# Kernel optimization log

Measured on AMD Instinct MI355X. Metric: run time of the kernel, lower is better.

Reference implementation:

```python
import jax, jax.numpy as jnp
import numpy as np

DIM_X = 128
DIM_H = 128
HIDDEN = 512
BATCH = 4096


def _vf(x, h, t, W1, b1, W2, b2):
    # cfg vector field: 2-layer tanh MLP on concat([x, h, t]) -> (B, dim_x)
    B = x.shape[0]
    tcol = jnp.broadcast_to(jnp.reshape(t, (1, 1)), (B, 1)).astype(x.dtype)
    z = jnp.concatenate([x, h, tcol], axis=-1)  # (B, dim_x+dim_h+1)
    return jnp.tanh(z @ W1 + b1) @ W2 + b2  # (B, dim_x)


def _divergence(x, h, t, W1, b1, W2, b2):
    # Exact Jacobian trace: sum_i d v_i / d x_i, via dim_x forward-mode JVP
    # passes (replaces the torch per-dim reverse-mode autograd.grad loop).
    f = lambda xx: _vf(xx, h, t, W1, b1, W2, b2)
    dim = x.shape[1]

    def diag_i(i):
        e = jnp.zeros((dim,), x.dtype).at[i].set(1.0)
        _, tang = jax.jvp(f, (x,), (jnp.broadcast_to(e, x.shape),))  # (B, dim)
        return jnp.take(tang, i, axis=1)  # (B,)

    diag = jax.vmap(diag_i)(jnp.arange(dim))  # (dim, B)
    return jnp.sum(diag, axis=0)[:, None]  # (B, 1)


def setup_inputs() -> dict:
    key = jax.random.key(0)
    ks = jax.random.split(key, 9)
    return {
        "state": jax.random.normal(ks[0], (BATCH, DIM_X + 1), jnp.float32),
        "h": jax.random.normal(ks[1], (BATCH, DIM_H), jnp.float32),
        "h_null": jax.random.normal(ks[2], (BATCH, DIM_H), jnp.float32),
        "t": jax.random.uniform(ks[3], (1,), jnp.float32),
        "guidance_scale": jax.random.uniform(ks[4], (1,), jnp.float32),
        "W1": jax.random.normal(ks[5], (DIM_X + DIM_H + 1, HIDDEN), jnp.float32) * 0.05,
        "b1": jax.random.normal(ks[6], (HIDDEN,), jnp.float32) * 0.05,
        "W2": jax.random.normal(ks[7], (HIDDEN, DIM_X), jnp.float32) * 0.05,
        "b2": jax.random.normal(ks[8], (DIM_X,), jnp.float32) * 0.05,
    }


def reference(state, h, h_null, t, guidance_scale, W1, b1, W2, b2):
    x_t = state[:, :-1]  # (B, dim_x)
    gs = guidance_scale[0]
    v_h = _vf(x_t, h, t, W1, b1, W2, b2)
    v_h_null = _vf(x_t, h_null, t, W1, b1, W2, b2)
    v = (1.0 - gs) * v_h_null + gs * v_h
    div_h = _divergence(x_t, h, t, W1, b1, W2, b2)
    div_h_null = _divergence(x_t, h_null, t, W1, b1, W2, b2)
    div = (1.0 - gs) * div_h_null + gs * div_h
    return jnp.concatenate([v, div], axis=1)  # (B, dim_x+1)
```

## Files before the change

### kernel.cpp

```cpp
#include <hip/hip_runtime.h>
#include <hip/hip_bf16.h>

#define DX 128
#define DH 128
#define HID 512
#define NB 4096
#define ROWS 16
#define OUTC 129

typedef __attribute__((ext_vector_type(4))) float f32x4;
typedef __attribute__((ext_vector_type(2))) float float2v;
typedef __attribute__((ext_vector_type(8))) short bf16x8;
typedef __attribute__((ext_vector_type(2))) short bf16x2;

__device__ inline short f2bf(float f) {
    unsigned u = __float_as_uint(f);
    unsigned r = (u + 0x7fffu + ((u >> 16) & 1u)) >> 16;
    return (short)r;
}

__device__ inline float fast_tanh(float x) {
    float e = __expf(2.0f * x);
    float r = __builtin_amdgcn_rcpf(e + 1.0f);
    return 1.0f - 2.0f * r;
}

__global__ __launch_bounds__(256) void prep_kernel(
    const float* __restrict__ W1, const float* __restrict__ W2,
    float* __restrict__ c, short* __restrict__ w1p, short* __restrict__ w2p)
{
    __shared__ float tile[4][32][17];

    const int tid  = threadIdx.x;
    const int lane = tid & 63;
    const int w    = tid >> 6;
    const int l15  = lane & 15;
    const int l4   = lane >> 4;
    const int W    = blockIdx.x * 4 + w;

    if (W < 256) {
        int nt = W >> 3, ks = W & 7;
        int m0 = ks * 32, n0 = nt * 16;
        #pragma unroll
        for (int p = 0; p < 8; ++p) {
            int r = p * 4 + l4;
            tile[w][r][l15] = W1[(m0 + r) * HID + n0 + l15];
        }
    } else if (W < 384) {
        int idx = W - 256;
        int nt = idx >> 4, ks = idx & 15;
        int k0 = ks * 32, n0 = nt * 16;
        #pragma unroll
        for (int p = 0; p < 8; ++p) {
            int r = p * 4 + l4;
            tile[w][r][l15] = W2[(k0 + r) * DX + n0 + l15];
        }
    }
    __syncthreads();

    if (W < 256) {
        bf16x8 v;
        #pragma unroll
        for (int e = 0; e < 8; ++e) v[e] = f2bf(tile[w][l4 * 8 + e][l15]);
        *(bf16x8*)&w1p[W * 512 + lane * 8] = v;
    } else if (W < 384) {
        int idx = W - 256;
        bf16x8 v;
        #pragma unroll
        for (int e = 0; e < 8; ++e) v[e] = f2bf(tile[w][l4 * 8 + e][l15]);
        *(bf16x8*)&w2p[idx * 512 + lane * 8] = v;
    } else if (W < 896) {
        int k = W - 384;
        float p = W1[lane * HID + k] * W2[k * DX + lane]
                + W1[(lane + 64) * HID + k] * W2[k * DX + lane + 64];
        for (int m = 1; m < 64; m <<= 1) p += __shfl_xor(p, m, 64);
        if (lane == 0) c[k] = p;
    }
}

__global__ __launch_bounds__(1024) void cvf_kernel(
    const float* __restrict__ state, const float* __restrict__ h_,
    const float* __restrict__ hn_, const float* __restrict__ tptr,
    const float* __restrict__ gsptr, const float* __restrict__ W1,
    const float* __restrict__ b1, const float* __restrict__ b2,
    const float* __restrict__ c, const short* __restrict__ w1p,
    const short* __restrict__ w2p, float* __restrict__ out)
{
    __shared__ short xb [ROWS][DX  + 8];
    __shared__ short hb [ROWS][DH  + 8];
    __shared__ short hnb[ROWS][DH  + 8];
    __shared__ short ab_h[ROWS][HID + 8];
    __shared__ short ab_n[ROWS][HID + 8];
    __shared__ float divp[2][16][ROWS];
    __shared__ float red[8][2][64][4];

    const int tid  = threadIdx.x;
    const int lane = tid & 63;
    const int w    = tid >> 6;
    const int l15  = lane & 15;
    const int l4   = lane >> 4;
    const int row0 = blockIdx.x * ROWS;
    const float t  = tptr[0];
    const float gs = gsptr[0];

    bf16x8 bx[2][4];
    float base[2];
    #pragma unroll
    for (int j = 0; j < 2; ++j) {
        #pragma unroll
        for (int ks = 0; ks < 4; ++ks)
            bx[j][ks] = *(const bf16x8*)&w1p[(((w * 2 + j) * 8 + ks) * 64 + lane) * 8];
        int k = w * 32 + j * 16 + l15;
        base[j] = b1[k] + t * W1[256 * HID + k];
    }

    {
        int r  = tid >> 6;
        int c0 = (tid & 63) * 2;
        const float* sp = state + (row0 + r) * OUTC + c0;
        float2v vh = *(const float2v*)(h_  + (row0 + r) * DH + c0);
        float2v vn = *(const float2v*)(hn_ + (row0 + r) * DH + c0);
        bf16x2 sx, sh, sn;
        for (int e = 0; e < 2; ++e) {
            sx[e] = f2bf(sp[e]);
            sh[e] = f2bf(vh[e]);
            sn[e] = f2bf(vn[e]);
        }
        *(bf16x2*)&xb [r][c0] = sx;
        *(bf16x2*)&hb [r][c0] = sh;
        *(bf16x2*)&hnb[r][c0] = sn;
    }
    __syncthreads();

    f32x4 acc_h[2], acc_n[2];
    {
        bf16x8 ax[4];
        #pragma unroll
        for (int ks = 0; ks < 4; ++ks)
            ax[ks] = *(const bf16x8*)&xb[l15][ks * 32 + l4 * 8];

        f32x4 accx[2];
        #pragma unroll
        for (int j = 0; j < 2; ++j)
            accx[j] = (f32x4){base[j], base[j], base[j], base[j]};
        #pragma unroll
        for (int ks = 0; ks < 4; ++ks)
            #pragma unroll
            for (int j = 0; j < 2; ++j)
                accx[j] = __builtin_amdgcn_mfma_f32_16x16x32_bf16(ax[ks], bx[j][ks], accx[j], 0, 0, 0);

        bf16x8 bh[2][4];
        #pragma unroll
        for (int j = 0; j < 2; ++j)
            #pragma unroll
            for (int ks = 0; ks < 4; ++ks)
                bh[j][ks] = *(const bf16x8*)&w1p[(((w * 2 + j) * 8 + 4 + ks) * 64 + lane) * 8];
        bf16x8 ah[4], an[4];
        #pragma unroll
        for (int ks = 0; ks < 4; ++ks) {
            ah[ks] = *(const bf16x8*)&hb [l15][ks * 32 + l4 * 8];
            an[ks] = *(const bf16x8*)&hnb[l15][ks * 32 + l4 * 8];
        }

        #pragma unroll
        for (int j = 0; j < 2; ++j) { acc_h[j] = accx[j]; acc_n[j] = accx[j]; }
        #pragma unroll
        for (int ks = 0; ks < 4; ++ks)
            #pragma unroll
            for (int j = 0; j < 2; ++j) {
                acc_h[j] = __builtin_amdgcn_mfma_f32_16x16x32_bf16(ah[ks], bh[j][ks], acc_h[j], 0, 0, 0);
                acc_n[j] = __builtin_amdgcn_mfma_f32_16x16x32_bf16(an[ks], bh[j][ks], acc_n[j], 0, 0, 0);
            }
    }

    const int nt2 = w >> 1;
    const int ks0 = (w & 1) * 8;
    bf16x8 b2f[8];
    #pragma unroll
    for (int ks = 0; ks < 8; ++ks)
        b2f[ks] = *(const bf16x8*)&w2p[((nt2 * 16 + ks0 + ks) * 64 + lane) * 8];

    float dph[4] = {0, 0, 0, 0}, dpn[4] = {0, 0, 0, 0};
    for (int j = 0; j < 2; ++j) {
        int k = w * 32 + j * 16 + l15;
        float ck = c[k];
        for (int q = 0; q < 4; ++q) {
            int r = l4 * 4 + q;
            float a1 = fast_tanh(acc_h[j][q]);
            float a2 = fast_tanh(acc_n[j][q]);
            ab_h[r][k] = f2bf(a1);
            ab_n[r][k] = f2bf(a2);
            dph[q] += (1.f - a1 * a1) * ck;
            dpn[q] += (1.f - a2 * a2) * ck;
        }
    }
    for (int q = 0; q < 4; ++q) {
        for (int m = 1; m < 16; m <<= 1) {
            dph[q] += __shfl_xor(dph[q], m, 64);
            dpn[q] += __shfl_xor(dpn[q], m, 64);
        }
    }
    if (l15 == 0) {
        for (int q = 0; q < 4; ++q) {
            divp[0][w][l4 * 4 + q] = dph[q];
            divp[1][w][l4 * 4 + q] = dpn[q];
        }
    }
    __syncthreads();

    f32x4 avh = (f32x4){0, 0, 0, 0}, avn = (f32x4){0, 0, 0, 0};
    #pragma unroll
    for (int ks = 0; ks < 8; ++ks) {
        bf16x8 afh = *(const bf16x8*)&ab_h[l15][(ks0 + ks) * 32 + l4 * 8];
        bf16x8 afn = *(const bf16x8*)&ab_n[l15][(ks0 + ks) * 32 + l4 * 8];
        avh = __builtin_amdgcn_mfma_f32_16x16x32_bf16(afh, b2f[ks], avh, 0, 0, 0);
        avn = __builtin_amdgcn_mfma_f32_16x16x32_bf16(afn, b2f[ks], avn, 0, 0, 0);
    }
    if (w & 1) {
        for (int q = 0; q < 4; ++q) {
            red[w >> 1][0][lane][q] = avh[q];
            red[w >> 1][1][lane][q] = avn[q];
        }
    }
    __syncthreads();

    if (!(w & 1)) {
        int col = (w >> 1) * 16 + l15;
        float bb = b2[col];
        for (int q = 0; q < 4; ++q) {
            int r = l4 * 4 + q;
            float vh = avh[q] + red[w >> 1][0][lane][q];
            float vn = avn[q] + red[w >> 1][1][lane][q];
            float v = (1.f - gs) * vn + gs * vh + bb;
            out[(row0 + r) * OUTC + col] = v;
        }
    }

    if (tid < ROWS) {
        float dh = 0.f, dn = 0.f;
        for (int ww = 0; ww < 16; ++ww) { dh += divp[0][ww][tid]; dn += divp[1][ww][tid]; }
        out[(row0 + tid) * OUTC + DX] = (1.f - gs) * dn + gs * dh;
    }
}

extern "C" void kernel_launch(void* const* d_in, const int* in_sizes, int n_in,
                              void* d_out, int out_size, void* d_ws, size_t ws_size,
                              hipStream_t stream) {
    const float* state = (const float*)d_in[0];
    const float* h     = (const float*)d_in[1];
    const float* hn    = (const float*)d_in[2];
    const float* t     = (const float*)d_in[3];
    const float* gs    = (const float*)d_in[4];
    const float* W1    = (const float*)d_in[5];
    const float* b1    = (const float*)d_in[6];
    const float* W2    = (const float*)d_in[7];
    const float* b2    = (const float*)d_in[8];
    float* out = (float*)d_out;

    float* c   = (float*)d_ws;
    short* w1p = (short*)((char*)d_ws + 2048);
    short* w2p = (short*)((char*)d_ws + 2048 + 262144);

    prep_kernel<<<224, 256, 0, stream>>>(W1, W2, c, w1p, w2p);
    cvf_kernel<<<NB / ROWS, 1024, 0, stream>>>(state, h, hn, t, gs, W1, b1, b2, c, w1p, w2p, out);
}
```

Before: 18.51 us.

## Transpose first-layer MFMA output and drop split-K reduction in second layer

```diff
diff --git a/kernel.cpp b/kernel.cpp
--- a/kernel.cpp
+++ b/kernel.cpp
@@ -9,8 +9,10 @@
 #define OUTC 129
 
 typedef __attribute__((ext_vector_type(4))) float f32x4;
+typedef __attribute__((ext_vector_type(4))) float float4v;
 typedef __attribute__((ext_vector_type(2))) float float2v;
 typedef __attribute__((ext_vector_type(8))) short bf16x8;
+typedef __attribute__((ext_vector_type(4))) short bf16x4;
 typedef __attribute__((ext_vector_type(2))) short bf16x2;
 
 __device__ inline short f2bf(float f) {
@@ -92,7 +94,6 @@
     __shared__ short ab_h[ROWS][HID + 8];
     __shared__ short ab_n[ROWS][HID + 8];
     __shared__ float divp[2][16][ROWS];
-    __shared__ float red[8][2][64][4];
 
     const int tid  = threadIdx.x;
     const int lane = tid & 63;
@@ -104,14 +105,17 @@
     const float gs = gsptr[0];
 
     bf16x8 bx[2][4];
-    float base[2];
+    f32x4 base[2];
     #pragma unroll
     for (int j = 0; j < 2; ++j) {
         #pragma unroll
         for (int ks = 0; ks < 4; ++ks)
             bx[j][ks] = *(const bf16x8*)&w1p[(((w * 2 + j) * 8 + ks) * 64 + lane) * 8];
-        int k = w * 32 + j * 16 + l15;
-        base[j] = b1[k] + t * W1[256 * HID + k];
+        int k0 = w * 32 + j * 16 + l4 * 4;
+        float4v bb = *(const float4v*)&b1[k0];
+        float4v tw = *(const float4v*)&W1[256 * HID + k0];
+        #pragma unroll
+        for (int q = 0; q < 4; ++q) base[j][q] = bb[q] + t * tw[q];
     }
 
     {
@@ -141,13 +145,12 @@
 
         f32x4 accx[2];
         #pragma unroll
-        for (int j = 0; j < 2; ++j)
-            accx[j] = (f32x4){base[j], base[j], base[j], base[j]};
+        for (int j = 0; j < 2; ++j) accx[j] = base[j];
         #pragma unroll
         for (int ks = 0; ks < 4; ++ks)
             #pragma unroll
             for (int j = 0; j < 2; ++j)
-                accx[j] = __builtin_amdgcn_mfma_f32_16x16x32_bf16(ax[ks], bx[j][ks], accx[j], 0, 0, 0);
+                accx[j] = __builtin_amdgcn_mfma_f32_16x16x32_bf16(bx[j][ks], ax[ks], accx[j], 0, 0, 0);
 
         bf16x8 bh[2][4];
         #pragma unroll
@@ -168,78 +171,77 @@
         for (int ks = 0; ks < 4; ++ks)
             #pragma unroll
             for (int j = 0; j < 2; ++j) {
-                acc_h[j] = __builtin_amdgcn_mfma_f32_16x16x32_bf16(ah[ks], bh[j][ks], acc_h[j], 0, 0, 0);
-                acc_n[j] = __builtin_amdgcn_mfma_f32_16x16x32_bf16(an[ks], bh[j][ks], acc_n[j], 0, 0, 0);
+                acc_h[j] = __builtin_amdgcn_mfma_f32_16x16x32_bf16(bh[j][ks], ah[ks], acc_h[j], 0, 0, 0);
+                acc_n[j] = __builtin_amdgcn_mfma_f32_16x16x32_bf16(bh[j][ks], an[ks], acc_n[j], 0, 0, 0);
             }
     }
 
-    const int nt2 = w >> 1;
-    const int ks0 = (w & 1) * 8;
     bf16x8 b2f[8];
+    if (w < 8) {
+        #pragma unroll
+        for (int ks = 0; ks < 8; ++ks)
+            b2f[ks] = *(const bf16x8*)&w2p[((w * 16 + ks) * 64 + lane) * 8];
+    }
+
+    float dph = 0.f, dpn = 0.f;
     #pragma unroll
-    for (int ks = 0; ks < 8; ++ks)
-        b2f[ks] = *(const bf16x8*)&w2p[((nt2 * 16 + ks0 + ks) * 64 + lane) * 8];
-
-    float dph[4] = {0, 0, 0, 0}, dpn[4] = {0, 0, 0, 0};
     for (int j = 0; j < 2; ++j) {
-        int k = w * 32 + j * 16 + l15;
-        float ck = c[k];
+        int k0 = w * 32 + j * 16 + l4 * 4;
+        float4v c4 = *(const float4v*)&c[k0];
+        bf16x4 ph, pn;
+        #pragma unroll
+        for (int q = 0; q < 4; ++q) {
+            float a1 = fast_tanh(acc_h[j][q]);
+            float a2 = fast_tanh(acc_n[j][q]);
+            ph[q] = f2bf(a1);
+            pn[q] = f2bf(a2);
+            dph += (1.f - a1 * a1) * c4[q];
+            dpn += (1.f - a2 * a2) * c4[q];
+        }
+        *(bf16x4*)&ab_h[l15][k0] = ph;
+        *(bf16x4*)&ab_n[l15][k0] = pn;
+    }
+    dph += __shfl_xor(dph, 16, 64);  dph += __shfl_xor(dph, 32, 64);
+    dpn += __shfl_xor(dpn, 16, 64);  dpn += __shfl_xor(dpn, 32, 64);
+    if (l4 == 0) {
+        divp[0][w][l15] = dph;
+        divp[1][w][l15] = dpn;
+    }
+    __syncthreads();
+
+    if (w < 8) {
+        f32x4 avh = (f32x4){0, 0, 0, 0}, avn = (f32x4){0, 0, 0, 0};
+        #pragma unroll
+        for (int ks = 0; ks < 8; ++ks) {
+            bf16x8 afh = *(const bf16x8*)&ab_h[l15][ks * 32 + l4 * 8];
+            bf16x8 afn = *(const bf16x8*)&ab_n[l15][ks * 32 + l4 * 8];
+            avh = __builtin_amdgcn_mfma_f32_16x16x32_bf16(afh, b2f[ks], avh, 0, 0, 0);
+            avn = __builtin_amdgcn_mfma_f32_16x16x32_bf16(afn, b2f[ks], avn, 0, 0, 0);
+        }
+        bf16x8 b2g[8];
+        #pragma unroll
+        for (int ks = 0; ks < 8; ++ks)
+            b2g[ks] = *(const bf16x8*)&w2p[((w * 16 + 8 + ks) * 64 + lane) * 8];
+        #pragma unroll
+        for (int ks = 0; ks < 8; ++ks) {
+            bf16x8 afh = *(const bf16x8*)&ab_h[l15][(8 + ks) * 32 + l4 * 8];
+            bf16x8 afn = *(const bf16x8*)&ab_n[l15][(8 + ks) * 32 + l4 * 8];
+            avh = __builtin_amdgcn_mfma_f32_16x16x32_bf16(afh, b2g[ks], avh, 0, 0, 0);
+            avn = __builtin_amdgcn_mfma_f32_16x16x32_bf16(afn, b2g[ks], avn, 0, 0, 0);
+        }
+        int col = w * 16 + l15;
+        float bb = b2[col];
+        #pragma unroll
         for (int q = 0; q < 4; ++q) {
             int r = l4 * 4 + q;
-            float a1 = fast_tanh(acc_h[j][q]);
-            float a2 = fast_tanh(acc_n[j][q]);
-            ab_h[r][k] = f2bf(a1);
-            ab_n[r][k] = f2bf(a2);
-            dph[q] += (1.f - a1 * a1) * ck;
-            dpn[q] += (1.f - a2 * a2) * ck;
-        }
-    }
-    for (int q = 0; q < 4; ++q) {
-        for (int m = 1; m < 16; m <<= 1) {
-            dph[q] += __shfl_xor(dph[q], m, 64);
-            dpn[q] += __shfl_xor(dpn[q], m, 64);
-        }
-    }
-    if (l15 == 0) {
-        for (int q = 0; q < 4; ++q) {
-            divp[0][w][l4 * 4 + q] = dph[q];
-            divp[1][w][l4 * 4 + q] = dpn[q];
-        }
-    }
-    __syncthreads();
-
-    f32x4 avh = (f32x4){0, 0, 0, 0}, avn = (f32x4){0, 0, 0, 0};
-    #pragma unroll
-    for (int ks = 0; ks < 8; ++ks) {
-        bf16x8 afh = *(const bf16x8*)&ab_h[l15][(ks0 + ks) * 32 + l4 * 8];
-        bf16x8 afn = *(const bf16x8*)&ab_n[l15][(ks0 + ks) * 32 + l4 * 8];
-        avh = __builtin_amdgcn_mfma_f32_16x16x32_bf16(afh, b2f[ks], avh, 0, 0, 0);
-        avn = __builtin_amdgcn_mfma_f32_16x16x32_bf16(afn, b2f[ks], avn, 0, 0, 0);
-    }
-    if (w & 1) {
-        for (int q = 0; q < 4; ++q) {
-            red[w >> 1][0][lane][q] = avh[q];
-            red[w >> 1][1][lane][q] = avn[q];
-        }
-    }
-    __syncthreads();
-
-    if (!(w & 1)) {
-        int col = (w >> 1) * 16 + l15;
-        float bb = b2[col];
-        for (int q = 0; q < 4; ++q) {
-            int r = l4 * 4 + q;
-            float vh = avh[q] + red[w >> 1][0][lane][q];
-            float vn = avn[q] + red[w >> 1][1][lane][q];
-            float v = (1.f - gs) * vn + gs * vh + bb;
+            float v = (1.f - gs) * avn[q] + gs * avh[q] + bb;
             out[(row0 + r) * OUTC + col] = v;
         }
-    }
-
-    if (tid < ROWS) {
+    } else if (w == 8 && lane < ROWS) {
         float dh = 0.f, dn = 0.f;
-        for (int ww = 0; ww < 16; ++ww) { dh += divp[0][ww][tid]; dn += divp[1][ww][tid]; }
-        out[(row0 + tid) * OUTC + DX] = (1.f - gs) * dn + gs * dh;
+        #pragma unroll
+        for (int ww = 0; ww < 16; ++ww) { dh += divp[0][ww][lane]; dn += divp[1][ww][lane]; }
+        out[(row0 + lane) * OUTC + DX] = (1.f - gs) * dn + gs * dh;
     }
 }
 
```

Result: no change. 18.75 us (+1.3%).
